# Kernel optimization log

Hardware: AMD Instinct MI355X
Metric: run time of the kernel (lower is better)

The kernel has to match this reference:

```python
import jax, jax.numpy as jnp
import numpy as np

THRESHOLD = 0.5
ALPHA = 1.0
N, D = 100000, 256
B, K = 1024, 128


def _l2norm(x):
    # F.normalize(x, p=2, dim=-1) with eps=1e-12
    return x / jnp.maximum(jnp.linalg.norm(x, axis=-1, keepdims=True), 1e-12)


def setup_inputs() -> dict:
    key = jax.random.key(0)
    k1, k2, k3, k4, k5, k6, k7 = jax.random.split(key, 7)
    feature = jax.random.normal(k1, (N, D), dtype=jnp.float32)
    text_embedding = jax.random.normal(k2, (N, D), dtype=jnp.float32)
    virtual = jax.random.normal(k3, (1, D), dtype=jnp.float32)
    # Gumbel(0,1) noise for gumbel_softmax (tau=1), materialized for determinism
    u = jax.random.uniform(k4, (B, K, K), dtype=jnp.float32, minval=1e-6, maxval=1.0 - 1e-6)
    gumbel = -jnp.log(-jnp.log(u))
    ego_nodes = jnp.sort(jax.random.randint(k5, (B, K), 0, N, dtype=jnp.int32), axis=-1)
    edges_adj = jax.random.randint(k6, (B, K, K), 0, 2, dtype=jnp.int32)
    train_label = jax.random.randint(k7, (B,), 0, 2, dtype=jnp.int32)
    return {"feature": feature, "text_embedding": text_embedding, "virtual": virtual,
            "gumbel": gumbel, "ego_nodes": ego_nodes, "edges_adj": edges_adj,
            "train_label": train_label}


def reference(feature, text_embedding, virtual, gumbel, ego_nodes, edges_adj, train_label):
    feat = _l2norm(feature)          # self.feature (normalized in __init__)
    emb = _l2norm(text_embedding)    # self.embedding
    te_local = _l2norm(emb - virtual)            # [N, D]

    tb = te_local[ego_nodes]                     # [B, K, D] gather per ego-subgraph
    sim = jnp.einsum('bkd,bjd->bkj', tb, tb) - THRESHOLD   # [B, K, K]
    sim_sub = jax.nn.softmax(sim + gumbel, axis=-1)         # gumbel_softmax, tau=1

    adj = edges_adj.astype(sim_sub.dtype)        # scatter edges_adj[src,dst]=1, precomputed
    # s_diff: row-wise L2 norm then mean over rows
    s_diff = jnp.sqrt(jnp.sum((adj - sim_sub) ** 2, axis=-1)).mean(axis=-1)   # [B]

    emb_out = feat[ego_nodes].mean(axis=1)       # [B, D] sum(feature)/n
    emb_pg = emb[ego_nodes].mean(axis=1)         # [B, D] sum(embedding)/n  (n == K)
    f_diff = jnp.linalg.norm(emb_out - emb_pg, axis=-1)                        # [B]

    score = s_diff + ALPHA * f_diff
    score = (score - score.min()) / (score.max() - score.min())

    y = train_label.astype(score.dtype)
    eps = 1e-7  # stabilizes log at exact 0/1 (torch BCELoss clamps log at -100)
    sc = jnp.clip(score, eps, 1.0 - eps)
    bce = -(y * jnp.log(sc) + (1.0 - y) * jnp.log1p(-sc)).mean()
    loss = bce / y.shape[0]
    return score, loss
```

## Files before the change

kernel.cpp:

```cpp
#include <hip/hip_runtime.h>
#include <hip/hip_bf16.h>
#include <math.h>

#define DIM 256
#define BB 1024
#define KK 128
#define PITCH 264

typedef __attribute__((ext_vector_type(8))) short short8;
typedef __attribute__((ext_vector_type(4))) float float4v;

__device__ __forceinline__ float dot4(const float4 a, const float4 b) {
    return a.x*b.x + a.y*b.y + a.z*b.z + a.w*b.w;
}

__device__ __forceinline__ unsigned bf2bits(float a, float b) {
    float2 t; t.x = a; t.y = b;
    __hip_bfloat162 h = __float22bfloat162_rn(t);
    unsigned u; __builtin_memcpy(&u, &h, 4);
    return u;
}

__global__ __launch_bounds__(1024, 8) void fused_main(
    const float* __restrict__ feature,
    const float* __restrict__ text,
    const float* __restrict__ virt,
    const float* __restrict__ gumbel,
    const int*   __restrict__ ego,
    const int*   __restrict__ adj,
    float*       __restrict__ score_raw)
{
    __shared__ unsigned short tbs[KK * PITCH];
    __shared__ float fpart8[8][DIM];
    __shared__ float rowpart[KK][8];
    __shared__ float spart[2];

    const int b    = blockIdx.x;
    const int tid  = threadIdx.x;
    const int wave = tid >> 6;
    const int lane = tid & 63;

    const int* ego_b = ego + b * KK;

    const float4 vm = ((const float4*)virt)[lane];
    float vv2 = dot4(vm, vm);
    #pragma unroll
    for (int m = 1; m < 64; m <<= 1) vv2 += __shfl_xor(vv2, m);

    const int baseA = wave * 8;
    int eidx[8];
    #pragma unroll
    for (int k = 0; k < 8; ++k) eidx[k] = ego_b[baseA + k];

    float4 fdv = make_float4(0.f, 0.f, 0.f, 0.f);

    float4 pt[2], pf[2];
    #pragma unroll
    for (int p = 0; p < 2; ++p) {
        pt[p] = ((const float4*)(text    + (size_t)eidx[p] * DIM))[lane];
        pf[p] = ((const float4*)(feature + (size_t)eidx[p] * DIM))[lane];
    }

    #pragma unroll
    for (int k = 0; k < 8; ++k) {
        const int sl = k & 1;
        const float4 ct = pt[sl], cf = pf[sl];
        if (k < 6) {
            pt[sl] = ((const float4*)(text    + (size_t)eidx[k+2] * DIM))[lane];
            pf[sl] = ((const float4*)(feature + (size_t)eidx[k+2] * DIM))[lane];
        }

        float st = dot4(ct, ct), sf = dot4(cf, cf), sv = dot4(ct, vm);
        #pragma unroll
        for (int m = 1; m < 64; m <<= 1) {
            st += __shfl_xor(st, m);
            sf += __shfl_xor(sf, m);
            sv += __shfl_xor(sv, m);
        }

        const float inv_ne = __builtin_amdgcn_rsqf(fmaxf(st, 1e-24f));
        const float inv_nf = __builtin_amdgcn_rsqf(fmaxf(sf, 1e-24f));
        const float nw2    = fmaxf(1.f + vv2 - 2.f * sv * inv_ne, 1e-24f);
        const float inv_nt = __builtin_amdgcn_rsqf(nw2);

        const float e0 = ct.x * inv_ne, e1 = ct.y * inv_ne;
        const float e2 = ct.z * inv_ne, e3 = ct.w * inv_ne;
        fdv.x += cf.x * inv_nf - e0;
        fdv.y += cf.y * inv_nf - e1;
        fdv.z += cf.z * inv_nf - e2;
        fdv.w += cf.w * inv_nf - e3;

        uint2 pk;
        pk.x = bf2bits((e0 - vm.x) * inv_nt, (e1 - vm.y) * inv_nt);
        pk.y = bf2bits((e2 - vm.z) * inv_nt, (e3 - vm.w) * inv_nt);
        *(uint2*)&tbs[(baseA + k) * PITCH + 4 * lane] = pk;
    }

    if (wave & 1) *(float4*)&fpart8[wave >> 1][4 * lane] = fdv;

    __syncthreads();

    if (!(wave & 1)) {
        float4 o = *(float4*)&fpart8[wave >> 1][4 * lane];
        o.x += fdv.x; o.y += fdv.y; o.z += fdv.z; o.w += fdv.w;
        *(float4*)&fpart8[wave >> 1][4 * lane] = o;
    }

    const int strip = wave >> 1;
    const int half  = wave & 1;
    const int g     = lane >> 4;
    const int c     = lane & 15;
    const int baseR = strip * 16;

    const float* gb = gumbel + (size_t)b * KK * KK;
    float gvv[16];
    #pragma unroll
    for (int r = 0; r < 4; ++r) {
        const float* gr = gb + (baseR + g*4 + r) * KK + half*64 + c;
        #pragma unroll
        for (int t = 0; t < 4; ++t)
            gvv[r*4 + t] = __builtin_nontemporal_load(gr + t*16);
    }

    float4v acc[4];
    const float4v zero = {0.f, 0.f, 0.f, 0.f};
    #pragma unroll
    for (int t = 0; t < 4; ++t) acc[t] = zero;

    #pragma unroll
    for (int q = 0; q < 8; ++q) {
        const int dq = q * 32 + g * 8;
        const short8 afr = *(const short8*)&tbs[(baseR + c) * PITCH + dq];
        #pragma unroll
        for (int t = 0; t < 4; ++t) {
            const short8 bfr = *(const short8*)&tbs[(half*64 + t*16 + c) * PITCH + dq];
            acc[t] = __builtin_amdgcn_mfma_f32_16x16x32_bf16(afr, bfr, acc[t], 0, 0, 0);
        }
    }

    const int* ab = adj + (size_t)b * KK * KK;
    unsigned am = 0;
    #pragma unroll
    for (int r = 0; r < 4; ++r) {
        const int* ar = ab + (baseR + g*4 + r) * KK + half*64 + c;
        #pragma unroll
        for (int t = 0; t < 4; ++t)
            am |= (__builtin_nontemporal_load(ar + t*16) ? 1u : 0u) << (r*4 + t);
    }

    #pragma unroll
    for (int r = 0; r < 4; ++r) {
        const unsigned mr = (am >> (r*4)) & 0xFu;
        float s = 0.f, a2 = 0.f, a3 = 0.f;
        #pragma unroll
        for (int t = 0; t < 4; ++t) {
            const float vt = acc[t][r] - 0.5f + gvv[r*4 + t];
            const float et = __expf(vt);
            s  += et;
            a3 += et * et;
            a2 += ((mr >> t) & 1u) ? et : 0.f;
        }
        float fia = (float)__popc(mr);
        #pragma unroll
        for (int msk = 1; msk < 16; msk <<= 1) {
            s   += __shfl_xor(s,   msk);
            a2  += __shfl_xor(a2,  msk);
            a3  += __shfl_xor(a3,  msk);
            fia += __shfl_xor(fia, msk);
        }
        if (c == 0) {
            float4 pk4; pk4.x = s; pk4.y = a2; pk4.z = a3; pk4.w = fia;
            *(float4*)&rowpart[baseR + g*4 + r][half * 4] = pk4;
        }
    }

    __syncthreads();

    if (tid < KK) {
        const float4 pa = *(const float4*)&rowpart[tid][0];
        const float4 pb = *(const float4*)&rowpart[tid][4];
        const float s   = pa.x + pb.x;
        const float a2  = pa.y + pb.y;
        const float a3  = pa.z + pb.z;
        const float fia = pa.w + pb.w;
        const float invS = __builtin_amdgcn_rcpf(s);
        float sq = sqrtf(fmaxf(fia - invS * (2.f * a2 - invS * a3), 0.f));
        #pragma unroll
        for (int m = 1; m < 64; m <<= 1) sq += __shfl_xor(sq, m);
        if (lane == 0) spart[wave] = sq;
    }

    __syncthreads();

    if (wave == 0) {
        float4 d = make_float4(0.f, 0.f, 0.f, 0.f);
        #pragma unroll
        for (int j = 0; j < 8; ++j) {
            const float4 p = *(const float4*)&fpart8[j][4 * lane];
            d.x += p.x; d.y += p.y; d.z += p.z; d.w += p.w;
        }
        const float inv = 1.f / 128.f;
        d.x *= inv; d.y *= inv; d.z *= inv; d.w *= inv;
        float q2 = dot4(d, d);
        #pragma unroll
        for (int m = 1; m < 64; m <<= 1) q2 += __shfl_xor(q2, m);
        if (lane == 0)
            score_raw[b] = (spart[0] + spart[1]) * (1.f / 128.f) + sqrtf(q2);
    }
}

__global__ __launch_bounds__(1024) void finalize(
    const float* __restrict__ score_raw,
    const int*   __restrict__ label,
    float*       __restrict__ out)
{
    __shared__ float wmin[16], wmax[16], wsum[16];
    const int tid = threadIdx.x;
    const float s = score_raw[tid];
    float mn = s, mx = s;
    #pragma unroll
    for (int m = 1; m < 64; m <<= 1) {
        mn = fminf(mn, __shfl_xor(mn, m));
        mx = fmaxf(mx, __shfl_xor(mx, m));
    }
    if ((tid & 63) == 0) { wmin[tid >> 6] = mn; wmax[tid >> 6] = mx; }
    __syncthreads();
    float gmn = wmin[0], gmx = wmax[0];
    #pragma unroll
    for (int w = 1; w < 16; ++w) {
        gmn = fminf(gmn, wmin[w]);
        gmx = fmaxf(gmx, wmax[w]);
    }
    const float score = (s - gmn) / (gmx - gmn);
    out[tid] = score;

    const float y  = (float)label[tid];
    const float sc = fminf(fmaxf(score, 1e-7f), 1.f - 1e-7f);
    float term = -(y * logf(sc) + (1.f - y) * log1pf(-sc));
    #pragma unroll
    for (int m = 1; m < 64; m <<= 1) term += __shfl_xor(term, m);
    if ((tid & 63) == 0) wsum[tid >> 6] = term;
    __syncthreads();
    if (tid == 0) {
        float tot = 0.f;
        #pragma unroll
        for (int w = 0; w < 16; ++w) tot += wsum[w];
        out[BB] = tot / (1024.f * 1024.f);
    }
}

extern "C" void kernel_launch(void* const* d_in, const int* in_sizes, int n_in,
                              void* d_out, int out_size, void* d_ws, size_t ws_size,
                              hipStream_t stream) {
    const float* feature = (const float*)d_in[0];
    const float* text    = (const float*)d_in[1];
    const float* virt    = (const float*)d_in[2];
    const float* gumbel  = (const float*)d_in[3];
    const int*   ego     = (const int*)d_in[4];
    const int*   adj     = (const int*)d_in[5];
    const int*   label   = (const int*)d_in[6];
    float* out       = (float*)d_out;
    float* score_raw = (float*)d_ws;

    fused_main<<<BB, 1024, 0, stream>>>(feature, text, virt, gumbel, ego, adj, score_raw);
    finalize<<<1, 1024, 0, stream>>>(score_raw, label, out);
}
```

Before: 76.03 us.

## Warp-specialize fused kernel into gather producer and MFMA consumer pipeline

Each block now handles four ego-subgraphs. Eight waves gather, normalize and pack the next subgraph into a double-buffered LDS tile while the other eight run the MFMA similarity and gumbel-softmax statistics for the previous one, and wave 0 finalizes the score two stages behind. The padded LDS pitch is replaced by an XOR swizzle, and feature-diff partials are stored as bf16. The aim is to overlap global gather latency with compute across subgraphs, at the cost of 4x fewer blocks (256 on the device), idle waves in each pipeline phase, and slightly lower precision in the f_diff partials.

```diff
diff --git a/kernel.cpp b/kernel.cpp
--- a/kernel.cpp
+++ b/kernel.cpp
@@ -5,7 +5,7 @@
 #define DIM 256
 #define BB 1024
 #define KK 128
-#define PITCH 264
+#define EPB 4
 
 typedef __attribute__((ext_vector_type(8))) short short8;
 typedef __attribute__((ext_vector_type(4))) float float4v;
@@ -20,193 +20,211 @@
     unsigned u; __builtin_memcpy(&u, &h, 4);
     return u;
 }
-
-__global__ __launch_bounds__(1024, 8) void fused_main(
-    const float* __restrict__ feature,
-    const float* __restrict__ text,
-    const float* __restrict__ virt,
-    const float* __restrict__ gumbel,
-    const int*   __restrict__ ego,
-    const int*   __restrict__ adj,
-    float*       __restrict__ score_raw)
+__device__ __forceinline__ float bf2f(unsigned short v) {
+    unsigned u = ((unsigned)v) << 16;
+    float f; __builtin_memcpy(&f, &u, 4);
+    return f;
+}
+
+__device__ __forceinline__ int swz(int row, int col) {
+    return (row << 8) + (col ^ ((row & 7) << 3));
+}
+
+__device__ __forceinline__ void score_one(const float* rp, const unsigned short* fp,
+                                          int lane, float* out)
 {
-    __shared__ unsigned short tbs[KK * PITCH];
-    __shared__ float fpart8[8][DIM];
-    __shared__ float rowpart[KK][8];
-    __shared__ float spart[2];
-
-    const int b    = blockIdx.x;
-    const int tid  = threadIdx.x;
-    const int wave = tid >> 6;
-    const int lane = tid & 63;
-
-    const int* ego_b = ego + b * KK;
-
-    const float4 vm = ((const float4*)virt)[lane];
-    float vv2 = dot4(vm, vm);
-    #pragma unroll
-    for (int m = 1; m < 64; m <<= 1) vv2 += __shfl_xor(vv2, m);
-
-    const int baseA = wave * 8;
-    int eidx[8];
-    #pragma unroll
-    for (int k = 0; k < 8; ++k) eidx[k] = ego_b[baseA + k];
-
-    float4 fdv = make_float4(0.f, 0.f, 0.f, 0.f);
-
-    float4 pt[2], pf[2];
-    #pragma unroll
-    for (int p = 0; p < 2; ++p) {
-        pt[p] = ((const float4*)(text    + (size_t)eidx[p] * DIM))[lane];
-        pf[p] = ((const float4*)(feature + (size_t)eidx[p] * DIM))[lane];
-    }
-
-    #pragma unroll
-    for (int k = 0; k < 8; ++k) {
-        const int sl = k & 1;
-        const float4 ct = pt[sl], cf = pf[sl];
-        if (k < 6) {
-            pt[sl] = ((const float4*)(text    + (size_t)eidx[k+2] * DIM))[lane];
-            pf[sl] = ((const float4*)(feature + (size_t)eidx[k+2] * DIM))[lane];
-        }
-
-        float st = dot4(ct, ct), sf = dot4(cf, cf), sv = dot4(ct, vm);
-        #pragma unroll
-        for (int m = 1; m < 64; m <<= 1) {
-            st += __shfl_xor(st, m);
-            sf += __shfl_xor(sf, m);
-            sv += __shfl_xor(sv, m);
-        }
-
-        const float inv_ne = __builtin_amdgcn_rsqf(fmaxf(st, 1e-24f));
-        const float inv_nf = __builtin_amdgcn_rsqf(fmaxf(sf, 1e-24f));
-        const float nw2    = fmaxf(1.f + vv2 - 2.f * sv * inv_ne, 1e-24f);
-        const float inv_nt = __builtin_amdgcn_rsqf(nw2);
-
-        const float e0 = ct.x * inv_ne, e1 = ct.y * inv_ne;
-        const float e2 = ct.z * inv_ne, e3 = ct.w * inv_ne;
-        fdv.x += cf.x * inv_nf - e0;
-        fdv.y += cf.y * inv_nf - e1;
-        fdv.z += cf.z * inv_nf - e2;
-        fdv.w += cf.w * inv_nf - e3;
-
-        uint2 pk;
-        pk.x = bf2bits((e0 - vm.x) * inv_nt, (e1 - vm.y) * inv_nt);
-        pk.y = bf2bits((e2 - vm.z) * inv_nt, (e3 - vm.w) * inv_nt);
-        *(uint2*)&tbs[(baseA + k) * PITCH + 4 * lane] = pk;
-    }
-
-    if (wave & 1) *(float4*)&fpart8[wave >> 1][4 * lane] = fdv;
-
-    __syncthreads();
-
-    if (!(wave & 1)) {
-        float4 o = *(float4*)&fpart8[wave >> 1][4 * lane];
-        o.x += fdv.x; o.y += fdv.y; o.z += fdv.z; o.w += fdv.w;
-        *(float4*)&fpart8[wave >> 1][4 * lane] = o;
-    }
-
-    const int strip = wave >> 1;
-    const int half  = wave & 1;
-    const int g     = lane >> 4;
-    const int c     = lane & 15;
-    const int baseR = strip * 16;
-
-    const float* gb = gumbel + (size_t)b * KK * KK;
-    float gvv[16];
-    #pragma unroll
-    for (int r = 0; r < 4; ++r) {
-        const float* gr = gb + (baseR + g*4 + r) * KK + half*64 + c;
-        #pragma unroll
-        for (int t = 0; t < 4; ++t)
-            gvv[r*4 + t] = __builtin_nontemporal_load(gr + t*16);
-    }
-
-    float4v acc[4];
-    const float4v zero = {0.f, 0.f, 0.f, 0.f};
-    #pragma unroll
-    for (int t = 0; t < 4; ++t) acc[t] = zero;
-
-    #pragma unroll
-    for (int q = 0; q < 8; ++q) {
-        const int dq = q * 32 + g * 8;
-        const short8 afr = *(const short8*)&tbs[(baseR + c) * PITCH + dq];
-        #pragma unroll
-        for (int t = 0; t < 4; ++t) {
-            const short8 bfr = *(const short8*)&tbs[(half*64 + t*16 + c) * PITCH + dq];
-            acc[t] = __builtin_amdgcn_mfma_f32_16x16x32_bf16(afr, bfr, acc[t], 0, 0, 0);
-        }
-    }
-
-    const int* ab = adj + (size_t)b * KK * KK;
-    unsigned am = 0;
-    #pragma unroll
-    for (int r = 0; r < 4; ++r) {
-        const int* ar = ab + (baseR + g*4 + r) * KK + half*64 + c;
-        #pragma unroll
-        for (int t = 0; t < 4; ++t)
-            am |= (__builtin_nontemporal_load(ar + t*16) ? 1u : 0u) << (r*4 + t);
-    }
-
-    #pragma unroll
-    for (int r = 0; r < 4; ++r) {
-        const unsigned mr = (am >> (r*4)) & 0xFu;
-        float s = 0.f, a2 = 0.f, a3 = 0.f;
-        #pragma unroll
-        for (int t = 0; t < 4; ++t) {
-            const float vt = acc[t][r] - 0.5f + gvv[r*4 + t];
-            const float et = __expf(vt);
-            s  += et;
-            a3 += et * et;
-            a2 += ((mr >> t) & 1u) ? et : 0.f;
-        }
-        float fia = (float)__popc(mr);
-        #pragma unroll
-        for (int msk = 1; msk < 16; msk <<= 1) {
-            s   += __shfl_xor(s,   msk);
-            a2  += __shfl_xor(a2,  msk);
-            a3  += __shfl_xor(a3,  msk);
-            fia += __shfl_xor(fia, msk);
-        }
-        if (c == 0) {
-            float4 pk4; pk4.x = s; pk4.y = a2; pk4.z = a3; pk4.w = fia;
-            *(float4*)&rowpart[baseR + g*4 + r][half * 4] = pk4;
-        }
-    }
-
-    __syncthreads();
-
-    if (tid < KK) {
-        const float4 pa = *(const float4*)&rowpart[tid][0];
-        const float4 pb = *(const float4*)&rowpart[tid][4];
+    float stot = 0.f;
+    #pragma unroll
+    for (int rr = 0; rr < 2; ++rr) {
+        const int row = lane * 2 + rr;
+        const float4 pa = *(const float4*)(rp + row * 8);
+        const float4 pb = *(const float4*)(rp + row * 8 + 4);
         const float s   = pa.x + pb.x;
         const float a2  = pa.y + pb.y;
         const float a3  = pa.z + pb.z;
         const float fia = pa.w + pb.w;
         const float invS = __builtin_amdgcn_rcpf(s);
-        float sq = sqrtf(fmaxf(fia - invS * (2.f * a2 - invS * a3), 0.f));
-        #pragma unroll
-        for (int m = 1; m < 64; m <<= 1) sq += __shfl_xor(sq, m);
-        if (lane == 0) spart[wave] = sq;
-    }
-
-    __syncthreads();
-
-    if (wave == 0) {
-        float4 d = make_float4(0.f, 0.f, 0.f, 0.f);
-        #pragma unroll
-        for (int j = 0; j < 8; ++j) {
-            const float4 p = *(const float4*)&fpart8[j][4 * lane];
-            d.x += p.x; d.y += p.y; d.z += p.z; d.w += p.w;
+        stot += sqrtf(fmaxf(fia - invS * (2.f * a2 - invS * a3), 0.f));
+    }
+    float4 d = make_float4(0.f, 0.f, 0.f, 0.f);
+    #pragma unroll
+    for (int j = 0; j < 8; ++j) {
+        const ushort4 u = *(const ushort4*)(fp + j * DIM + 4 * lane);
+        d.x += bf2f(u.x); d.y += bf2f(u.y);
+        d.z += bf2f(u.z); d.w += bf2f(u.w);
+    }
+    const float inv = 1.f / 128.f;
+    d.x *= inv; d.y *= inv; d.z *= inv; d.w *= inv;
+    float q2 = dot4(d, d);
+    #pragma unroll
+    for (int m = 1; m < 64; m <<= 1) {
+        stot += __shfl_xor(stot, m);
+        q2   += __shfl_xor(q2,   m);
+    }
+    if (lane == 0) *out = stot * (1.f / 128.f) + sqrtf(q2);
+}
+
+__global__ __attribute__((amdgpu_flat_work_group_size(1024, 1024),
+                          amdgpu_waves_per_eu(4, 4)))
+void fused_main(const float* __restrict__ feature,
+                const float* __restrict__ text,
+                const float* __restrict__ virt,
+                const float* __restrict__ gumbel,
+                const int*   __restrict__ ego,
+                const int*   __restrict__ adj,
+                float*       __restrict__ score_raw)
+{
+    __shared__ unsigned short tbs[2][KK * DIM];
+    __shared__ float rowpart[2][KK][8];
+    __shared__ unsigned short fpart[3][8][DIM];
+
+    const int tid  = threadIdx.x;
+    const int wave = tid >> 6;
+    const int lane = tid & 63;
+    const int b0   = blockIdx.x * EPB;
+    const int g    = lane >> 4;
+    const int c    = lane & 15;
+
+    const float4 vm = ((const float4*)virt)[lane];
+    float vv2 = dot4(vm, vm);
+    #pragma unroll
+    for (int m = 1; m < 64; m <<= 1) vv2 += __shfl_xor(vv2, m);
+
+    #pragma unroll
+    for (int i = 0; i <= EPB; ++i) {
+        if (wave < 8) {
+            if (i >= 2 && wave == 0)
+                score_one(&rowpart[(i - 2) & 1][0][0], &fpart[(i - 2) % 3][0][0],
+                          lane, &score_raw[b0 + i - 2]);
+
+            if (i >= 1) {
+                const int e = b0 + (i - 1);
+                const unsigned short* tb = &tbs[(i - 1) & 1][0];
+                float* rp = &rowpart[(i - 1) & 1][0][0];
+                const int base = wave * 16;
+                const float* gr = gumbel + ((size_t)e * KK + base + g * 4) * KK + c;
+                const int*   ar = adj    + ((size_t)e * KK + base + g * 4) * KK + c;
+
+                #pragma unroll
+                for (int h = 0; h < 2; ++h) {
+                    int a_in[4]; float g_in[4];
+                    #pragma unroll
+                    for (int t = 0; t < 4; ++t) {
+                        a_in[t] = __builtin_nontemporal_load(ar + h * 64 + t * 16);
+                        g_in[t] = __builtin_nontemporal_load(gr + h * 64 + t * 16);
+                    }
+                    float4v acc[4];
+                    #pragma unroll
+                    for (int t = 0; t < 4; ++t) acc[t] = (float4v){0.f, 0.f, 0.f, 0.f};
+                    #pragma unroll
+                    for (int q = 0; q < 8; ++q) {
+                        const int dq = q * 32 + g * 8;
+                        const short8 afr = *(const short8*)&tb[swz(base + c, dq)];
+                        #pragma unroll
+                        for (int t = 0; t < 4; ++t) {
+                            const short8 bfr =
+                                *(const short8*)&tb[swz(h * 64 + t * 16 + c, dq)];
+                            acc[t] = __builtin_amdgcn_mfma_f32_16x16x32_bf16(
+                                afr, bfr, acc[t], 0, 0, 0);
+                        }
+                    }
+                    #pragma unroll
+                    for (int r = 0; r < 4; ++r) {
+                        int av[4]; float gv[4];
+                        #pragma unroll
+                        for (int t = 0; t < 4; ++t) { av[t] = a_in[t]; gv[t] = g_in[t]; }
+                        if (r < 3) {
+                            #pragma unroll
+                            for (int t = 0; t < 4; ++t) {
+                                a_in[t] = __builtin_nontemporal_load(
+                                    ar + (r + 1) * KK + h * 64 + t * 16);
+                                g_in[t] = __builtin_nontemporal_load(
+                                    gr + (r + 1) * KK + h * 64 + t * 16);
+                            }
+                        }
+                        float s = 0.f, a2 = 0.f, a3 = 0.f, fia = 0.f;
+                        #pragma unroll
+                        for (int t = 0; t < 4; ++t) {
+                            const float vt = acc[t][r] - 0.5f + gv[t];
+                            const float et = __expf(vt);
+                            s  += et;
+                            a3 += et * et;
+                            a2 += av[t] ? et : 0.f;
+                            fia += av[t] ? 1.f : 0.f;
+                        }
+                        #pragma unroll
+                        for (int m = 1; m < 16; m <<= 1) {
+                            s   += __shfl_xor(s,   m);
+                            a2  += __shfl_xor(a2,  m);
+                            a3  += __shfl_xor(a3,  m);
+                            fia += __shfl_xor(fia, m);
+                        }
+                        if (c == 0) {
+                            float4 pk; pk.x = s; pk.y = a2; pk.z = a3; pk.w = fia;
+                            *(float4*)(rp + (base + g * 4 + r) * 8 + h * 4) = pk;
+                        }
+                    }
+                }
+            }
+        } else {
+            if (i < EPB) {
+                const int e  = b0 + i;
+                const int gw = wave - 8;
+                unsigned short* tb = &tbs[i & 1][0];
+                const int* ego_b = ego + (size_t)e * KK + gw * 16;
+                int eidx[16];
+                #pragma unroll
+                for (int k = 0; k < 16; ++k) eidx[k] = ego_b[k];
+
+                float4 fdv = make_float4(0.f, 0.f, 0.f, 0.f);
+                float4 pt[2], pf[2];
+                #pragma unroll
+                for (int p = 0; p < 2; ++p) {
+                    pt[p] = ((const float4*)(text    + (size_t)eidx[p] * DIM))[lane];
+                    pf[p] = ((const float4*)(feature + (size_t)eidx[p] * DIM))[lane];
+                }
+                #pragma unroll
+                for (int k = 0; k < 16; ++k) {
+                    const int sl = k & 1;
+                    const float4 ct = pt[sl], cf = pf[sl];
+                    if (k < 14) {
+                        pt[sl] = ((const float4*)(text    + (size_t)eidx[k + 2] * DIM))[lane];
+                        pf[sl] = ((const float4*)(feature + (size_t)eidx[k + 2] * DIM))[lane];
+                    }
+                    float st = dot4(ct, ct), sf = dot4(cf, cf), sv = dot4(ct, vm);
+                    #pragma unroll
+                    for (int m = 1; m < 64; m <<= 1) {
+                        st += __shfl_xor(st, m);
+                        sf += __shfl_xor(sf, m);
+                        sv += __shfl_xor(sv, m);
+                    }
+                    const float inv_ne = __builtin_amdgcn_rsqf(fmaxf(st, 1e-24f));
+                    const float inv_nf = __builtin_amdgcn_rsqf(fmaxf(sf, 1e-24f));
+                    const float nw2    = fmaxf(1.f + vv2 - 2.f * sv * inv_ne, 1e-24f);
+                    const float inv_nt = __builtin_amdgcn_rsqf(nw2);
+                    const float e0 = ct.x * inv_ne, e1 = ct.y * inv_ne;
+                    const float e2 = ct.z * inv_ne, e3 = ct.w * inv_ne;
+                    fdv.x += cf.x * inv_nf - e0;
+                    fdv.y += cf.y * inv_nf - e1;
+                    fdv.z += cf.z * inv_nf - e2;
+                    fdv.w += cf.w * inv_nf - e3;
+                    uint2 pk;
+                    pk.x = bf2bits((e0 - vm.x) * inv_nt, (e1 - vm.y) * inv_nt);
+                    pk.y = bf2bits((e2 - vm.z) * inv_nt, (e3 - vm.w) * inv_nt);
+                    *(uint2*)&tb[swz(gw * 16 + k, 4 * lane)] = pk;
+                }
+                uint2 fpk;
+                fpk.x = bf2bits(fdv.x, fdv.y);
+                fpk.y = bf2bits(fdv.z, fdv.w);
+                *(uint2*)&fpart[i % 3][gw][4 * lane] = fpk;
+            }
         }
-        const float inv = 1.f / 128.f;
-        d.x *= inv; d.y *= inv; d.z *= inv; d.w *= inv;
-        float q2 = dot4(d, d);
-        #pragma unroll
-        for (int m = 1; m < 64; m <<= 1) q2 += __shfl_xor(q2, m);
-        if (lane == 0)
-            score_raw[b] = (spart[0] + spart[1]) * (1.f / 128.f) + sqrtf(q2);
-    }
+        __syncthreads();
+    }
+
+    if (wave == 0)
+        score_one(&rowpart[(EPB - 1) & 1][0][0], &fpart[(EPB - 1) % 3][0][0],
+                  lane, &score_raw[b0 + EPB - 1]);
 }
 
 __global__ __launch_bounds__(1024) void finalize(
@@ -262,6 +280,7 @@
     float* out       = (float*)d_out;
     float* score_raw = (float*)d_ws;
 
-    fused_main<<<BB, 1024, 0, stream>>>(feature, text, virt, gumbel, ego, adj, score_raw);
+    fused_main<<<BB / EPB, 1024, 0, stream>>>(feature, text, virt, gumbel, ego, adj,
+                                              score_raw);
     finalize<<<1, 1024, 0, stream>>>(score_raw, label, out);
 }
```

New measurement: 79.59 us. +4.7%, slower.
